# Optimization experiments

Hardware: AMD Instinct MI355X
Metric: run time of the kernel (lower is better)

Reference implementation:

```python
import jax, jax.numpy as jnp
import numpy as np

EPS = 1e-5

def _ln(x, g, b):
    m = jnp.mean(x, axis=-1, keepdims=True)
    v = jnp.var(x, axis=-1, keepdims=True)
    return (x - m) / jnp.sqrt(v + EPS) * g + b

def _mha(q, k, v, Wqkv, bqkv, Wo, bo, nh):
    # torch nn.MultiheadAttention with packed in_proj: rows [0:D]=Q, [D:2D]=K, [2D:3D]=V
    D = q.shape[-1]; hd = D // nh
    qp = q @ Wqkv[:D].T + bqkv[:D]
    kp = k @ Wqkv[D:2 * D].T + bqkv[D:2 * D]
    vp = v @ Wqkv[2 * D:].T + bqkv[2 * D:]
    sh = lambda t: t.reshape(t.shape[0], t.shape[1], nh, hd).transpose(0, 2, 1, 3)
    scores = jnp.einsum('bhqd,bhkd->bhqk', sh(qp), sh(kp)) / np.float32(np.sqrt(hd))
    a = jax.nn.softmax(scores, axis=-1)
    o = jnp.einsum('bhqk,bhkd->bhqd', a, sh(vp)).transpose(0, 2, 1, 3).reshape(q.shape[0], q.shape[1], D)
    return o @ Wo.T + bo

def _forward(x, W_in, b_in, W_l, b_l, g_l, be_l, W_ih, W_hh, b_ih, b_hh, mem0,
             W_rh, b_rh, W_wh, b_wh, W_eh, b_eh, W_rg, b_rg, W_wg, b_wg,
             W_wm_qkv, b_wm_qkv, W_wm_o, b_wm_o, W_ca_qkv, b_ca_qkv, W_ca_o, b_ca_o,
             W_ai, b_ai, g_ca, be_ca, W_out, b_out):
    B, S, _ = x.shape
    H = W_in.shape[0]
    # input projection + residual MLP stack (eval mode: dropout is identity)
    h = x @ W_in.T + b_in
    for i in range(W_l.shape[0]):
        r = h
        h = _ln(jax.nn.relu(h @ W_l[i].T + b_l[i]), g_l[i], be_l[i])
        h = h + r  # use_residual=True
    # working-memory (NTM-style) scan over time
    Hd = H

    def step(carry, xt):
        hs, cs, mem = carry
        gates = xt @ W_ih.T + b_ih + hs @ W_hh.T + b_hh
        i_, f_, g_, o_ = jnp.split(gates, 4, axis=-1)  # torch LSTM gate order i,f,g,o
        cs = jax.nn.sigmoid(f_) * cs + jax.nn.sigmoid(i_) * jnp.tanh(g_)
        hs = jax.nn.sigmoid(o_) * jnp.tanh(cs)
        # read (attention over memory, then gate)
        rk = hs @ W_rh.T + b_rh
        ro = _mha(rk[:, None, :], mem, mem, W_wm_qkv, b_wm_qkv, W_wm_o, b_wm_o, 4)
        rg = jax.nn.sigmoid(hs @ W_rg.T + b_rg)  # [B,1]
        read = (rg[:, :, None] * ro)[:, 0]
        # write (erase + add with content-based addressing, unscaled bmm softmax)
        wp = hs @ W_wh.T + b_wh
        wk, wv = wp[:, :Hd], wp[:, Hd:]
        ev = jax.nn.sigmoid(hs @ W_eh.T + b_eh)
        wg = jax.nn.sigmoid(hs @ W_wg.T + b_wg)  # [B,1]
        att = jax.nn.softmax(jnp.einsum('bd,bmd->bm', wk, mem), axis=-1)
        ew = att[:, :, None]  # [B,M,1]
        mem = mem * (1.0 - ew * ev[:, None, :]) + wg[:, None, :] * (ew * wv[:, None, :])
        return (hs, cs, mem), xt + read

    mem_init = jnp.broadcast_to(mem0, (B,) + mem0.shape)
    init = (jnp.zeros((B, H), x.dtype), jnp.zeros((B, H), x.dtype), mem_init)
    _, outs = jax.lax.scan(step, init, h.transpose(1, 0, 2))
    wm = outs.transpose(1, 0, 2)  # [B,S,H]
    # cognitive attention, task_type='general' (no task modulation branch)
    att = _mha(wm, wm, wm, W_ca_qkv, b_ca_qkv, W_ca_o, b_ca_o, 8)
    inten = jax.nn.sigmoid(wm @ W_ai.T + b_ai)
    co = _ln(att * inten + wm, g_ca, be_ca)
    return co @ W_out.T + b_out

def setup_inputs():
    key = jax.random.key(0)
    ks = iter(jax.random.split(key, 40))
    B, S, DI, H, DO, L, M = 16, 512, 64, 128, 64, 3, 32
    w = lambda *s: jax.random.normal(next(ks), s, jnp.float32) * 0.05
    d = {}
    d['x'] = jax.random.normal(next(ks), (B, S, DI), jnp.float32)
    d['W_in'] = w(H, DI); d['b_in'] = jnp.zeros(H)
    d['W_l'] = w(L, H, H); d['b_l'] = jnp.zeros((L, H))
    d['g_l'] = jnp.ones((L, H)); d['be_l'] = jnp.zeros((L, H))
    d['W_ih'] = w(4 * H, H); d['W_hh'] = w(4 * H, H)
    d['b_ih'] = jnp.zeros(4 * H); d['b_hh'] = jnp.zeros(4 * H)
    d['mem0'] = w(M, H)
    d['W_rh'] = w(H, H); d['b_rh'] = jnp.zeros(H)
    d['W_wh'] = w(2 * H, H); d['b_wh'] = jnp.zeros(2 * H)
    d['W_eh'] = w(H, H); d['b_eh'] = jnp.zeros(H)
    d['W_rg'] = w(1, H); d['b_rg'] = jnp.zeros(1)
    d['W_wg'] = w(1, H); d['b_wg'] = jnp.zeros(1)
    d['W_wm_qkv'] = w(3 * H, H); d['b_wm_qkv'] = jnp.zeros(3 * H)
    d['W_wm_o'] = w(H, H); d['b_wm_o'] = jnp.zeros(H)
    d['W_ca_qkv'] = w(3 * H, H); d['b_ca_qkv'] = jnp.zeros(3 * H)
    d['W_ca_o'] = w(H, H); d['b_ca_o'] = jnp.zeros(H)
    d['W_ai'] = w(1, H); d['b_ai'] = jnp.zeros(1)
    d['g_ca'] = jnp.ones(H); d['be_ca'] = jnp.zeros(H)
    d['W_out'] = w(DO, H); d['b_out'] = jnp.zeros(DO)
    return d

def reference(x, W_in, b_in, W_l, b_l, g_l, be_l, W_ih, W_hh, b_ih, b_hh, mem0,
              W_rh, b_rh, W_wh, b_wh, W_eh, b_eh, W_rg, b_rg, W_wg, b_wg,
              W_wm_qkv, b_wm_qkv, W_wm_o, b_wm_o, W_ca_qkv, b_ca_qkv, W_ca_o, b_ca_o,
              W_ai, b_ai, g_ca, be_ca, W_out, b_out):
    return _forward(x, W_in, b_in, W_l, b_l, g_l, be_l, W_ih, W_hh, b_ih, b_hh, mem0,
                    W_rh, b_rh, W_wh, b_wh, W_eh, b_eh, W_rg, b_rg, W_wg, b_wg,
                    W_wm_qkv, b_wm_qkv, W_wm_o, b_wm_o, W_ca_qkv, b_ca_qkv, W_ca_o, b_ca_o,
                    W_ai, b_ai, g_ca, be_ca, W_out, b_out)
```

## Files before the change

### kernel.cpp

```cpp
#include <hip/hip_runtime.h>
#include <hip/hip_bf16.h>


typedef short bf16x8 __attribute__((ext_vector_type(8)));
typedef float f32x4 __attribute__((ext_vector_type(4)));

__device__ __forceinline__ float bl(uint u) { return __uint_as_float(u << 16); }
__device__ __forceinline__ float bh(uint u) { return __uint_as_float(u & 0xffff0000u); }
__device__ __forceinline__ float b2f(ushort u) { return __uint_as_float(((uint)u) << 16); }
__device__ __forceinline__ ushort f2b(float f) {
  uint u = __float_as_uint(f);
  u += 0x7fffu + ((u >> 16) & 1u);
  return (ushort)(u >> 16);
}
__device__ __forceinline__ float rdl(float v, int lane) {
  return __int_as_float(__builtin_amdgcn_readlane(__float_as_int(v), lane));
}
__device__ __forceinline__ float sigm(float x) { return 1.0f / (1.0f + __expf(-x)); }
__device__ __forceinline__ float tanh_(float x) { float e = __expf(2.0f * x); return 1.0f - 2.0f / (e + 1.0f); }

#define O_H     ((size_t)0)
#define O_GX    ((size_t)1048576)
#define O_QCA   ((size_t)1048576)
#define O_KCA   ((size_t)2097152)
#define O_VCA   ((size_t)3145728)
#define O_AO    ((size_t)4194304)
#define O_HS    ((size_t)5242880)
#define O_WM    ((size_t)5242880)
#define O_WK    ((size_t)6291456)
#define O_WV    ((size_t)7340032)
#define O_EV    ((size_t)8388608)
#define O_Q     ((size_t)9437184)
#define O_WGS   ((size_t)10485760)
#define O_RGS   ((size_t)10493952)
#define O_BQC   ((size_t)10502144)
#define O_MEMA  ((size_t)10502272)
#define O_PWIN  ((size_t)27279488)
#define O_PWL   ((size_t)27283584)
#define O_PWIH  ((size_t)27308160)
#define O_PCMB  ((size_t)27340928)
#define O_PQKV  ((size_t)27373696)
#define O_PWOC  ((size_t)27398272)
#define O_PWOUT ((size_t)27406464)
#define O_PWOWM ((size_t)27410688)
#define O_WQC16 ((size_t)27418880)
#define O_CAN   ((size_t)27427072)

#define F4LD(DST, OFS, P) { float4 _f = *(const float4*)(P); DST[(OFS)]=_f.x; DST[(OFS)+1]=_f.y; DST[(OFS)+2]=_f.z; DST[(OFS)+3]=_f.w; }

struct CV { const void* src; uint dst; uint n; };
struct CVA { CV d[36]; };
__global__ __launch_bounds__(256) void k_cvt(CVA a, ushort* cb)
{
  __shared__ int flag;
  int tid = threadIdx.x;
  const ushort* xu = (const ushort*)a.d[0].src;
  if (tid < 64) {
    int sane = 0;
    for (int i = tid; i < 512; i += 64) {
      int e = (xu[2 * i] >> 7) & 0xFF;
      sane += (e >= 0x70 && e <= 0x8E) ? 1 : 0;
    }
#pragma unroll
    for (int d = 1; d < 64; d <<= 1) sane += __shfl_xor(sane, d, 64);
    if (tid == 0) flag = (sane > 256) ? 0 : 1;
  }
  __syncthreads();
  int isf32 = flag;
  CV c = a.d[blockIdx.x];
  ushort* dst = cb + c.dst;
  uint start = blockIdx.y * 256 + tid, stride = gridDim.y * 256;
  if (isf32) {
    const float* s = (const float*)c.src;
    for (uint j = start; j < c.n; j += stride) dst[j] = f2b(s[j]);
  } else {
    const ushort* s = (const ushort*)c.src;
    for (uint j = start; j < c.n; j += stride) dst[j] = s[j];
  }
}

__global__ __launch_bounds__(256) void k_wqcomb(const ushort* __restrict__ Wqkv, const ushort* __restrict__ Wrh,
                                                const ushort* __restrict__ brh, const ushort* __restrict__ bqkv,
                                                ushort* __restrict__ wqc, float* __restrict__ bqc)
{
  __shared__ float qr[2][128];
  int tid = threadIdx.x;
  int r = tid >> 7, e = tid & 127;
  int j = blockIdx.x * 2 + r;
  qr[r][e] = b2f(Wqkv[j * 128 + e]);
  __syncthreads();
  float acc = 0.f;
  for (int k = 0; k < 128; ++k) acc += qr[r][k] * b2f(Wrh[k * 128 + e]);
  wqc[j * 128 + e] = f2b(acc);
  if (e == 0) {
    float s = 0.f;
    for (int k = 0; k < 128; ++k) s += qr[r][k] * b2f(brh[k]);
    bqc[j] = s + b2f(bqkv[j]);
  }
}

struct PD { const ushort* src; uint* dst; int R, C2, RT, base; };
struct PA { PD d[12]; };
__global__ __launch_bounds__(256) void k_pack(PA a)
{
  int p = blockIdx.x >> 5, sl = blockIdx.x & 31;
  PD q = a.d[p];
  for (int d2 = sl; d2 < q.C2; d2 += 32)
    for (int j = threadIdx.x; j < q.R; j += 256)
      q.dst[(size_t)d2 * q.RT + q.base + j] = *(const uint*)(q.src + (size_t)j * q.C2 * 2 + d2 * 2);
}

__device__ __forceinline__ void mlp_layer(float& h0, float& h1, const uint* wp, const float* bias, int li, int l)
{
  float t0 = bias[(1 + li) * 128 + l], t1 = bias[(1 + li) * 128 + 64 + l];
// ... 47 lines not shown
    for (int d2 = 0; d2 < 32; ++d2) {
      float s0 = rdl(xv, 2 * d2), s1 = rdl(xv, 2 * d2 + 1);
      uint u0 = lds[d2 * 128 + l], u1 = lds[d2 * 128 + 64 + l];
      h0 += s0 * bl(u0) + s1 * bh(u0);
      h1 += s0 * bl(u1) + s1 * bh(u1);
    }
    mlp_layer(h0, h1, lds + 4096, bias, 0, l);
    h0a[ps] = h0; h1a[ps] = h1;
  }
  __syncthreads();
  for (int i = tid; i < 8192; i += 256) lds[i] = pk[12288 + i];
  __syncthreads();
#pragma unroll
  for (int ps = 0; ps < 8; ++ps) {
    float h0 = h0a[ps], h1 = h1a[ps];
    mlp_layer(h0, h1, lds, bias, 1, l);
    h0a[ps] = h0; h1a[ps] = h1;
  }
  __syncthreads();
  for (int i = tid; i < 8192; i += 256) lds[i] = pk[20480 + i];
  __syncthreads();
#pragma unroll
  for (int ps = 0; ps < 8; ++ps) {
    int tok = blockIdx.x * 32 + ps * 4 + wv;
    float h0 = h0a[ps], h1 = h1a[ps];
    mlp_layer(h0, h1, lds, bias, 2, l);
    h_all[(size_t)tok * 128 + l] = h0;
    h_all[(size_t)tok * 128 + 64 + l] = h1;
  }
}

__global__ __launch_bounds__(256, 1) void k_gates(const float* __restrict__ h_all, const uint* __restrict__ pk,
    const ushort* __restrict__ b_ih, const ushort* __restrict__ b_hh, float* __restrict__ gx)
{
  __shared__ uint lds[8192];
  __shared__ float biasg[512];
  int tid = threadIdx.x;
  for (int i = tid; i < 512; i += 256) biasg[i] = b2f(b_ih[i]) + b2f(b_hh[i]);
  int wv = tid >> 6, l = tid & 63;
  for (int s = 0; s < 4; ++s) {
    __syncthreads();
    for (int i = tid; i < 8192; i += 256) { int d2 = i >> 7, j = i & 127; lds[i] = pk[d2 * 512 + s * 128 + j]; }
    __syncthreads();
    for (int ps = 0; ps < 8; ++ps) {
      int tok = blockIdx.x * 32 + ps * 4 + wv;
      float h0 = h_all[(size_t)tok * 128 + l], h1 = h_all[(size_t)tok * 128 + 64 + l];
      float a0 = biasg[s * 128 + l], a1 = biasg[s * 128 + 64 + l];
#pragma unroll
      for (int d2 = 0; d2 < 64; ++d2) {
        float s0 = rdl(d2 < 32 ? h0 : h1, (2 * d2) & 63);
        float s1 = rdl(d2 < 32 ? h0 : h1, (2 * d2 + 1) & 63);
        uint u0 = lds[d2 * 128 + l], u1 = lds[d2 * 128 + 64 + l];
        a0 += s0 * bl(u0) + s1 * bh(u0);
        a1 += s0 * bl(u1) + s1 * bh(u1);
      }
      gx[(size_t)tok * 512 + s * 128 + l] = a0;
      gx[(size_t)tok * 512 + s * 128 + 64 + l] = a1;
    }
  }
}

__global__ __launch_bounds__(512, 2) void k_lstm(const float* __restrict__ gx, const ushort* __restrict__ Whh,
                                                 float* __restrict__ hs_all)
{
  __shared__ float hsl[128];
  __shared__ float gact[512];
  int tid = threadIdx.x;
  int b = blockIdx.x;
  float2 w2[64];
  {
    const ushort* rp = Whh + (size_t)tid * 128;
#pragma unroll
    for (int q = 0; q < 16; ++q) {
      uint4 v = *(const uint4*)(rp + q * 8);
      w2[q * 4 + 0] = make_float2(bl(v.x), bh(v.x));
      w2[q * 4 + 1] = make_float2(bl(v.y), bh(v.y));
      w2[q * 4 + 2] = make_float2(bl(v.z), bh(v.z));
      w2[q * 4 + 3] = make_float2(bl(v.w), bh(v.w));
    }
  }
  if (tid < 128) hsl[tid] = 0.f;
  float cs = 0.f;
  const float* gbase = gx + (size_t)b * 512 * 512;
  float gcur = gbase[tid];
  int grp = tid >> 7;
  __syncthreads();
  for (int t = 0; t < 512; ++t) {
    float gnext = 0.f;
    if (t < 511) gnext = gbase[(size_t)(t + 1) * 512 + tid];
    float ax = gcur, ay = 0.f;
#pragma unroll
    for (int i = 0; i < 64; ++i) {
      float2 s2 = *(const float2*)(hsl + 2 * i);
      ax = fmaf(w2[i].x, s2.x, ax);
      ay = fmaf(w2[i].y, s2.y, ay);
    }
    float a = ax + ay;
    gact[tid] = (grp == 2) ? tanh_(a) : sigm(a);
    __syncthreads();
    if (tid < 128) {
      float si = gact[tid], sf = gact[128 + tid], tg = gact[256 + tid], so = gact[384 + tid];
      cs = sf * cs + si * tg;
      float hv = so * tanh_(cs);
      hsl[tid] = hv;
      hs_all[((size_t)b * 512 + t) * 128 + tid] = hv;
    }
    gcur = gnext;
    __syncthreads();
  }
}

__global__ __launch_bounds__(256, 1) void k_proj(const float* __restrict__ hs_all, const uint* __restrict__ pk,
    const ushort* __restrict__ bwh, const ushort* __restrict__ beh, const float* __restrict__ bqc,
    const ushort* __restrict__ wrg, const ushort* __restrict__ brg, const ushort* __restrict__ wwg,
    const ushort* __restrict__ bwg,
    float* __restrict__ wk_a, float* __restrict__ wv_a, float* __restrict__ ev_a, float* __restrict__ q_a,
    float* __restrict__ rg_a, float* __restrict__ wg_a)
{
  __shared__ uint lds[8192];
  __shared__ float biasc[512];
  int tid = threadIdx.x;
  for (int i = tid; i < 512; i += 256)
    biasc[i] = (i < 256) ? b2f(bwh[i]) : (i < 384) ? b2f(beh[i - 256]) : bqc[i - 384];
  float brgv = b2f(brg[0]), bwgv = b2f(bwg[0]);
  int wv = tid >> 6, l = tid & 63;
  for (int s = 0; s < 4; ++s) {
    __syncthreads();
    for (int i = tid; i < 8192; i += 256) { int d2 = i >> 7, j = i & 127; lds[i] = pk[d2 * 512 + s * 128 + j]; }
    __syncthreads();
    for (int ps = 0; ps < 8; ++ps) {
      int tok = blockIdx.x * 32 + ps * 4 + wv;
      float h0 = hs_all[(size_t)tok * 128 + l], h1 = hs_all[(size_t)tok * 128 + 64 + l];
      float a0 = biasc[s * 128 + l], a1 = biasc[s * 128 + 64 + l];
#pragma unroll
      for (int d2 = 0; d2 < 64; ++d2) {
        float s0 = rdl(d2 < 32 ? h0 : h1, (2 * d2) & 63);
        float s1 = rdl(d2 < 32 ? h0 : h1, (2 * d2 + 1) & 63);
        uint u0 = lds[d2 * 128 + l], u1 = lds[d2 * 128 + 64 + l];
        a0 += s0 * bl(u0) + s1 * bh(u0);
        a1 += s0 * bl(u1) + s1 * bh(u1);
      }
      if (s == 0) {
        wk_a[(size_t)tok * 128 + l] = a0;
        wk_a[(size_t)tok * 128 + 64 + l] = a1;
        float pr = h0 * b2f(wrg[l]) + h1 * b2f(wrg[64 + l]);
        float pw = h0 * b2f(wwg[l]) + h1 * b2f(wwg[64 + l]);
#pragma unroll
        for (int d = 1; d < 64; d <<= 1) { pr += __shfl_xor(pr, d, 64); pw += __shfl_xor(pw, d, 64); }
        if (l == 0) { rg_a[tok] = sigm(pr + brgv); wg_a[tok] = sigm(pw + bwgv); }
      } else if (s == 1) {
        wv_a[(size_t)tok * 128 + l] = a0;
        wv_a[(size_t)tok * 128 + 64 + l] = a1;
      } else if (s == 2) {
        ev_a[(size_t)tok * 128 + l] = sigm(a0);
        ev_a[(size_t)tok * 128 + 64 + l] = sigm(a1);
      } else {
        q_a[(size_t)tok * 128 + l] = a0;
        q_a[(size_t)tok * 128 + 64 + l] = a1;
      }
    }
  }
}

#define B2STEP(T, CK, CV, CE, CG, NK, NV, NE, NG) { \
    { uint p0 = (uint)f2b(mr[0]) | ((uint)f2b(mr[1]) << 16); \
      uint p1 = (uint)f2b(mr[2]) | ((uint)f2b(mr[3]) << 16); \
      uint p2 = (uint)f2b(mr[4]) | ((uint)f2b(mr[5]) << 16); \
      uint p3 = (uint)f2b(mr[6]) | ((uint)f2b(mr[7]) << 16); \
      uint p4 = (uint)f2b(mr[8]) | ((uint)f2b(mr[9]) << 16); \
      uint p5 = (uint)f2b(mr[10]) | ((uint)f2b(mr[11]) << 16); \
      uint p6 = (uint)f2b(mr[12]) | ((uint)f2b(mr[13]) << 16); \
      uint p7 = (uint)f2b(mr[14]) | ((uint)f2b(mr[15]) << 16); \
      uint4* d4 = (uint4*)(mb + (size_t)(T) * 2048); \
      d4[0] = make_uint4(p0, p1, p2, p3); \
      d4[1] = make_uint4(p4, p5, p6, p7); } \
    if ((T) + 1 < 512) { \
      size_t nb = base0 + (size_t)((T) + 1) * 128; \
      F4LD(NK, 0, wk_a + nb); F4LD(NK, 4, wk_a + nb + 4); F4LD(NK, 8, wk_a + nb + 8); F4LD(NK, 12, wk_a + nb + 12); \
      F4LD(NV, 0, wv_a + nb); F4LD(NV, 4, wv_a + nb + 4); F4LD(NV, 8, wv_a + nb + 8); F4LD(NV, 12, wv_a + nb + 12); \
      F4LD(NE, 0, ev_a + nb); F4LD(NE, 4, ev_a + nb + 4); F4LD(NE, 8, ev_a + nb + 8); F4LD(NE, 12, ev_a + nb + 12); \
      NG = wg_a[(size_t)b * 512 + (T) + 1]; } \
    float dp = 0.f; \
    _Pragma("unroll") for (int i = 0; i < 16; ++i) dp += CK[i] * mr[i]; \
    dp += __shfl_xor(dp, 1, 64); dp += __shfl_xor(dp, 2, 64); dp += __shfl_xor(dp, 4, 64); \
    float mx = dp; \
    mx = fmaxf(mx, __shfl_xor(mx, 8, 64)); mx = fmaxf(mx, __shfl_xor(mx, 16, 64)); mx = fmaxf(mx, __shfl_xor(mx, 32, 64)); \
    if (l == 0) red[w] = mx; \
    __syncthreads(); \
    mx = fmaxf(fmaxf(red[0], red[1]), fmaxf(red[2], red[3])); \
    float e = __expf(dp - mx); \
    float smv = e; \
    smv += __shfl_xor(smv, 8, 64); smv += __shfl_xor(smv, 16, 64); smv += __shfl_xor(smv, 32, 64); \
    if (l == 0) red[4 + w] = smv; \
    __syncthreads(); \
    float den = (red[4] + red[5]) + (red[6] + red[7]); \
    float ew = e / den; \
    float gw = (CG) * ew; \
    _Pragma("unroll") for (int i = 0; i < 16; ++i) mr[i] = mr[i] * (1.f - ew * CE[i]) + gw * CV[i]; \
  }

__global__ __launch_bounds__(256, 1) void k_memrec(const float* __restrict__ wk_a, const float* __restrict__ wv_a,
    const float* __restrict__ ev_a, const float* __restrict__ wg_a, const ushort* __restrict__ mem0,
    uint* __restrict__ mem_all)
{
  __shared__ float red[8];
  int tid = threadIdx.x, l = tid & 63, w = tid >> 6;
  int b = blockIdx.x;
  int m = tid >> 3, d0 = (tid & 7) * 16;
  float mr[16];
#pragma unroll
  for (int i = 0; i < 16; ++i) mr[i] = b2f(mem0[m * 128 + d0 + i]);
  float ck[16], cv[16], ce[16], cg;
  float nk[16], nv[16], ne[16], ng;
  ng = 0.f; cg = 0.f;
  size_t base0 = (size_t)b * 512 * 128 + d0;
  F4LD(ck, 0, wk_a + base0); F4LD(ck, 4, wk_a + base0 + 4); F4LD(ck, 8, wk_a + base0 + 8); F4LD(ck, 12, wk_a + base0 + 12);
  F4LD(cv, 0, wv_a + base0); F4LD(cv, 4, wv_a + base0 + 4); F4LD(cv, 8, wv_a + base0 + 8); F4LD(cv, 12, wv_a + base0 + 12);
  F4LD(ce, 0, ev_a + base0); F4LD(ce, 4, ev_a + base0 + 4); F4LD(ce, 8, ev_a + base0 + 8); F4LD(ce, 12, ev_a + base0 + 12);
  cg = wg_a[(size_t)b * 512];
  uint* mb = mem_all + (size_t)b * 512 * 2048 + tid * 8;
  for (int t = 0; t < 512; t += 2) {
    B2STEP(t, ck, cv, ce, cg, nk, nv, ne, ng);
    B2STEP(t + 1, nk, nv, ne, ng, ck, cv, ce, cg);
  }
}

__global__ __launch_bounds__(256, 1) void k_read(const ushort* __restrict__ Wqkv, const ushort* __restrict__ bwo,
    const uint* __restrict__ wo_pk, const uint* __restrict__ mem_all, const float* __restrict__ q_all,
    const float* __restrict__ rg_all, const float* __restrict__ h_all, float* __restrict__ wm_all)
{
  __shared__ float Kl[32 * 133];
  __shared__ float Vl[32 * 133];
  __shared__ __align__(16) char ml[8192];
  __shared__ float ql[128];
  __shared__ float ol[128];
  __shared__ float part[256];
  int tid = threadIdx.x, l = tid & 63, w = tid >> 6;
  int b = blockIdx.x >> 6, c = blockIdx.x & 63;
  int mat = w >> 1, chh = w & 1;
  bf16x8 bfr[4][4];
#pragma unroll
  for (int ct = 0; ct < 4; ++ct)
#pragma unroll
    for (int kt = 0; kt < 4; ++kt) {
      int j = chh * 64 + ct * 16 + (l & 15);
      bfr[ct][kt] = *(const bf16x8*)(Wqkv + (size_t)(128 + mat * 128 + j) * 128 + kt * 32 + (l >> 4) * 8);
    }
  for (int s8 = 0; s8 < 8; ++s8) {
    int t = c * 8 + s8;
    size_t bt = (size_t)b * 512 + t;
    {
      const uint4* src = (const uint4*)(mem_all + bt * 2048);
      uint4 v0 = src[tid * 2], v1 = src[tid * 2 + 1];
      int row = tid >> 3;
      int b0 = row * 256 + (tid & 7) * 32;
      int sw = (row & 7) << 4;
      *(uint4*)(ml + (b0 ^ sw)) = v0;
      *(uint4*)(ml + ((b0 + 16) ^ sw)) = v1;
    }
    if (tid < 128) ql[tid] = q_all[bt * 128 + tid];
    __syncthreads();
    f32x4 acc[2][4];
#pragma unroll
    for (int rt = 0; rt < 2; ++rt)
#pragma unroll
      for (int ct = 0; ct < 4; ++ct) { f32x4 z = {0.f, 0.f, 0.f, 0.f}; acc[rt][ct] = z; }
    bf16x8 af[2][4];
#pragma unroll
    for (int rt = 0; rt < 2; ++rt)
#pragma unroll
      for (int kt = 0; kt < 4; ++kt) {
        int row = rt * 16 + (l & 15);
        int byte0 = (row * 256 + kt * 64 + (l >> 4) * 16) ^ ((row & 7) << 4);
        af[rt][kt] = *(const bf16x8*)(ml + byte0);
      }
#pragma unroll
    for (int rt = 0; rt < 2; ++rt)
#pragma unroll
      for (int ct = 0; ct < 4; ++ct)
#pragma unroll
        for (int kt = 0; kt < 4; ++kt)
          acc[rt][ct] = __builtin_amdgcn_mfma_f32_16x16x32_bf16(af[rt][kt], bfr[ct][kt], acc[rt][ct], 0, 0, 0);
    {
      float* dst = mat ? Vl : Kl;
#pragma unroll
      for (int rt = 0; rt < 2; ++rt)
#pragma unroll
        for (int ct = 0; ct < 4; ++ct)
#pragma unroll
          for (int rr = 0; rr < 4; ++rr) {
            int row = rt * 16 + (l >> 4) * 4 + rr;
            int col = chh * 64 + ct * 16 + (l & 15);
            dst[row * 133 + col] = acc[rt][ct][rr];
          }
    }
    __syncthreads();
    {
      int hh = w;
      float qv[16];
#pragma unroll
      for (int q = 0; q < 4; ++q) { F4LD(qv, 4 * q, ql + hh * 32 + (l >> 5) * 16 + 4 * q); }
      int m = l & 31;
      float sv = 0.f;
#pragma unroll
      for (int i = 0; i < 16; ++i) sv += qv[i] * Kl[m * 133 + hh * 32 + (l >> 5) * 16 + i];
      sv += __shfl_xor(sv, 32, 64);
// ... 201 lines not shown
      float s1 = rdl(d2 < 32 ? c0 : c1, (2 * d2 + 1) & 63);
      uint u = lds[8192 + d2 * 64 + l];
      ob += s0 * bl(u) + s1 * bh(u);
    }
    out[(size_t)tok * 64 + l] = ob;
  }
}

extern "C" void kernel_launch(void* const* d_in, const int* in_sizes, int n_in,
                              void* d_out, int out_size, void* d_ws, size_t ws_size,
                              hipStream_t stream)
{
  (void)out_size; (void)ws_size;
  float* ws = (float*)d_ws;
  uint* wsu = (uint*)d_ws;
  ushort* cb = (ushort*)(wsu + O_CAN);

  uint off[36]; uint cum = 0;
  for (int i = 0; i < 36; ++i) { off[i] = cum; cum = (cum + (uint)in_sizes[i] + 7u) & ~7u; }

  CVA ca;
  for (int i = 0; i < 36; ++i) ca.d[i] = CV{ d_in[i], off[i], (uint)in_sizes[i] };
  k_cvt<<<dim3(36, 16), 256, 0, stream>>>(ca, cb);

  const ushort* x        = cb + off[0];
  const ushort* W_in     = cb + off[1];
  const ushort* b_in     = cb + off[2];
  const ushort* W_l      = cb + off[3];
  const ushort* b_l      = cb + off[4];
  const ushort* g_l      = cb + off[5];
  const ushort* be_l     = cb + off[6];
  const ushort* W_ih     = cb + off[7];
  const ushort* W_hh     = cb + off[8];
  const ushort* b_ih     = cb + off[9];
  const ushort* b_hh     = cb + off[10];
  const ushort* mem0     = cb + off[11];
  const ushort* W_rh     = cb + off[12];
  const ushort* b_rh     = cb + off[13];
  const ushort* W_wh     = cb + off[14];
  const ushort* b_wh     = cb + off[15];
  const ushort* W_eh     = cb + off[16];
  const ushort* b_eh     = cb + off[17];
  const ushort* W_rg     = cb + off[18];
  const ushort* b_rg     = cb + off[19];
  const ushort* W_wg     = cb + off[20];
  const ushort* b_wg     = cb + off[21];
  const ushort* W_wm_qkv = cb + off[22];
  const ushort* b_wm_qkv = cb + off[23];
  const ushort* W_wm_o   = cb + off[24];
  const ushort* b_wm_o   = cb + off[25];
  const ushort* W_ca_qkv = cb + off[26];
  const ushort* b_ca_qkv = cb + off[27];
  const ushort* W_ca_o   = cb + off[28];
  const ushort* b_ca_o   = cb + off[29];
  const ushort* W_ai     = cb + off[30];
  const ushort* b_ai     = cb + off[31];
  const ushort* g_ca     = cb + off[32];
  const ushort* be_ca    = cb + off[33];
  const ushort* W_out    = cb + off[34];
  const ushort* b_out    = cb + off[35];

  k_wqcomb<<<64, 256, 0, stream>>>(W_wm_qkv, W_rh, b_rh, b_wm_qkv, (ushort*)(wsu + O_WQC16), ws + O_BQC);

  PA pa;
  pa.d[0]  = PD{ W_in,                       wsu + O_PWIN,  128, 32, 128, 0 };
  pa.d[1]  = PD{ W_l,                        wsu + O_PWL,   128, 64, 128, 0 };
  pa.d[2]  = PD{ W_l + 16384,                wsu + O_PWL + 8192,  128, 64, 128, 0 };
  pa.d[3]  = PD{ W_l + 32768,                wsu + O_PWL + 16384, 128, 64, 128, 0 };
  pa.d[4]  = PD{ W_ih,                       wsu + O_PWIH,  512, 64, 512, 0 };
  pa.d[5]  = PD{ W_wh,                       wsu + O_PCMB,  256, 64, 512, 0 };
  pa.d[6]  = PD{ W_eh,                       wsu + O_PCMB,  128, 64, 512, 256 };
  pa.d[7]  = PD{ (const ushort*)(wsu + O_WQC16), wsu + O_PCMB, 128, 64, 512, 384 };
  pa.d[8]  = PD{ W_ca_qkv,                   wsu + O_PQKV,  384, 64, 384, 0 };
  pa.d[9]  = PD{ W_ca_o,                     wsu + O_PWOC,  128, 64, 128, 0 };
  pa.d[10] = PD{ W_out,                      wsu + O_PWOUT,  64, 64,  64, 0 };
  pa.d[11] = PD{ W_wm_o,                     wsu + O_PWOWM, 128, 64, 128, 0 };
  k_pack<<<384, 256, 0, stream>>>(pa);

  k_mlp<<<256, 256, 0, stream>>>(x, wsu + O_PWIN, b_in, b_l, g_l, be_l, ws + O_H);
  k_gates<<<256, 256, 0, stream>>>(ws + O_H, wsu + O_PWIH, b_ih, b_hh, ws + O_GX);
  k_lstm<<<16, 512, 0, stream>>>(ws + O_GX, W_hh, ws + O_HS);
  k_proj<<<256, 256, 0, stream>>>(ws + O_HS, wsu + O_PCMB, b_wh, b_eh, ws + O_BQC,
                                  W_rg, b_rg, W_wg, b_wg,
                                  ws + O_WK, ws + O_WV, ws + O_EV, ws + O_Q, ws + O_RGS, ws + O_WGS);
  k_memrec<<<16, 256, 0, stream>>>(ws + O_WK, ws + O_WV, ws + O_EV, ws + O_WGS, mem0, wsu + O_MEMA);
  k_read<<<1024, 256, 0, stream>>>(W_wm_qkv, b_wm_o, wsu + O_PWOWM, wsu + O_MEMA,
                                   ws + O_Q, ws + O_RGS, ws + O_H, ws + O_WM);
  k_caqkv<<<256, 256, 0, stream>>>(ws + O_WM, wsu + O_PQKV, b_ca_qkv, ws + O_QCA, ws + O_KCA, ws + O_VCA);
  k_caattn<<<256, 256, 0, stream>>>(ws + O_QCA, ws + O_KCA, ws + O_VCA, ws + O_AO);
  k_cafinal<<<256, 256, 0, stream>>>(ws + O_WM, ws + O_AO, wsu + O_PWOC, wsu + O_PWOUT,
                                     W_ai, b_ai, g_ca, be_ca, b_ca_o, b_out, (float*)d_out);
}
```

Before: 1.543 ms.

## Rewrite memory recurrence as single-wave kernel; batch LSTM hidden-state stores

The memory-update recurrence kernel moves from 256 threads with two block barriers per step to a single 64-lane wave. Each lane owns two feature columns across all 32 memory slots, uses a shuffle-based transpose reduction for the slot scores, and packs bf16 with a hardware convert instruction. This removes the per-step __syncthreads cost on the serial 512-step path, at the price of more work per lane and lower parallelism. The LSTM kernel also buffers eight hidden states and prefetches eight gate rows at a time, batching its global stores.

```diff
diff --git a/kernel.cpp b/kernel.cpp
--- a/kernel.cpp
+++ b/kernel.cpp
@@ -12,6 +12,11 @@
   uint u = __float_as_uint(f);
   u += 0x7fffu + ((u >> 16) & 1u);
   return (ushort)(u >> 16);
+}
+__device__ __forceinline__ uint cvtpk(float lo, float hi) {
+  uint r;
+  asm("v_cvt_pk_bf16_f32 %0, %1, %2" : "=v"(r) : "v"(lo), "v"(hi));
+  return r;
 }
 __device__ __forceinline__ float rdl(float v, int lane) {
   return __int_as_float(__builtin_amdgcn_readlane(__float_as_int(v), lane));
@@ -243,31 +248,44 @@
   if (tid < 128) hsl[tid] = 0.f;
   float cs = 0.f;
   const float* gbase = gx + (size_t)b * 512 * 512;
-  float gcur = gbase[tid];
   int grp = tid >> 7;
-  __syncthreads();
-  for (int t = 0; t < 512; ++t) {
-    float gnext = 0.f;
-    if (t < 511) gnext = gbase[(size_t)(t + 1) * 512 + tid];
-    float ax = gcur, ay = 0.f;
-#pragma unroll
-    for (int i = 0; i < 64; ++i) {
-      float2 s2 = *(const float2*)(hsl + 2 * i);
-      ax = fmaf(w2[i].x, s2.x, ax);
-      ay = fmaf(w2[i].y, s2.y, ay);
-    }
-    float a = ax + ay;
-    gact[tid] = (grp == 2) ? tanh_(a) : sigm(a);
-    __syncthreads();
+  float g8[8], g8n[8], hv8[8];
+#pragma unroll
+  for (int j = 0; j < 8; ++j) { g8[j] = gbase[(size_t)j * 512 + tid]; hv8[j] = 0.f; g8n[j] = 0.f; }
+  __syncthreads();
+  for (int tb = 0; tb < 512; tb += 8) {
+    if (tb + 8 < 512) {
+#pragma unroll
+      for (int j = 0; j < 8; ++j) g8n[j] = gbase[(size_t)(tb + 8 + j) * 512 + tid];
+    }
+#pragma unroll
+    for (int j = 0; j < 8; ++j) {
+      float ax = g8[j], ay = 0.f;
+#pragma unroll
+      for (int i = 0; i < 64; ++i) {
+        float2 s2 = *(const float2*)(hsl + 2 * i);
+        ax = fmaf(w2[i].x, s2.x, ax);
+        ay = fmaf(w2[i].y, s2.y, ay);
+      }
+      float a = ax + ay;
+      gact[tid] = (grp == 2) ? tanh_(a) : sigm(a);
+      __syncthreads();
+      if (tid < 128) {
+        float si = gact[tid], sf = gact[128 + tid], tg = gact[256 + tid], so = gact[384 + tid];
+        cs = sf * cs + si * tg;
+        float hv = so * tanh_(cs);
+        hsl[tid] = hv;
+        hv8[j] = hv;
+      }
+      __syncthreads();
+    }
     if (tid < 128) {
-      float si = gact[tid], sf = gact[128 + tid], tg = gact[256 + tid], so = gact[384 + tid];
-      cs = sf * cs + si * tg;
-      float hv = so * tanh_(cs);
-      hsl[tid] = hv;
-      hs_all[((size_t)b * 512 + t) * 128 + tid] = hv;
-    }
-    gcur = gnext;
-    __syncthreads();
+      float* hp = hs_all + ((size_t)b * 512 + tb) * 128 + tid;
+#pragma unroll
+      for (int j = 0; j < 8; ++j) hp[(size_t)j * 128] = hv8[j];
+    }
+#pragma unroll
+    for (int j = 0; j < 8; ++j) g8[j] = g8n[j];
   }
 }
 
@@ -323,66 +341,91 @@
   }
 }
 
-#define B2STEP(T, CK, CV, CE, CG, NK, NV, NE, NG) { \
-    { uint p0 = (uint)f2b(mr[0]) | ((uint)f2b(mr[1]) << 16); \
-      uint p1 = (uint)f2b(mr[2]) | ((uint)f2b(mr[3]) << 16); \
-      uint p2 = (uint)f2b(mr[4]) | ((uint)f2b(mr[5]) << 16); \
-      uint p3 = (uint)f2b(mr[6]) | ((uint)f2b(mr[7]) << 16); \
-      uint p4 = (uint)f2b(mr[8]) | ((uint)f2b(mr[9]) << 16); \
-      uint p5 = (uint)f2b(mr[10]) | ((uint)f2b(mr[11]) << 16); \
-      uint p6 = (uint)f2b(mr[12]) | ((uint)f2b(mr[13]) << 16); \
-      uint p7 = (uint)f2b(mr[14]) | ((uint)f2b(mr[15]) << 16); \
-      uint4* d4 = (uint4*)(mb + (size_t)(T) * 2048); \
-      d4[0] = make_uint4(p0, p1, p2, p3); \
-      d4[1] = make_uint4(p4, p5, p6, p7); } \
-    if ((T) + 1 < 512) { \
-      size_t nb = base0 + (size_t)((T) + 1) * 128; \
-      F4LD(NK, 0, wk_a + nb); F4LD(NK, 4, wk_a + nb + 4); F4LD(NK, 8, wk_a + nb + 8); F4LD(NK, 12, wk_a + nb + 12); \
-      F4LD(NV, 0, wv_a + nb); F4LD(NV, 4, wv_a + nb + 4); F4LD(NV, 8, wv_a + nb + 8); F4LD(NV, 12, wv_a + nb + 12); \
-      F4LD(NE, 0, ev_a + nb); F4LD(NE, 4, ev_a + nb + 4); F4LD(NE, 8, ev_a + nb + 8); F4LD(NE, 12, ev_a + nb + 12); \
-      NG = wg_a[(size_t)b * 512 + (T) + 1]; } \
-    float dp = 0.f; \
-    _Pragma("unroll") for (int i = 0; i < 16; ++i) dp += CK[i] * mr[i]; \
-    dp += __shfl_xor(dp, 1, 64); dp += __shfl_xor(dp, 2, 64); dp += __shfl_xor(dp, 4, 64); \
-    float mx = dp; \
-    mx = fmaxf(mx, __shfl_xor(mx, 8, 64)); mx = fmaxf(mx, __shfl_xor(mx, 16, 64)); mx = fmaxf(mx, __shfl_xor(mx, 32, 64)); \
-    if (l == 0) red[w] = mx; \
-    __syncthreads(); \
-    mx = fmaxf(fmaxf(red[0], red[1]), fmaxf(red[2], red[3])); \
-    float e = __expf(dp - mx); \
-    float smv = e; \
-    smv += __shfl_xor(smv, 8, 64); smv += __shfl_xor(smv, 16, 64); smv += __shfl_xor(smv, 32, 64); \
-    if (l == 0) red[4 + w] = smv; \
-    __syncthreads(); \
-    float den = (red[4] + red[5]) + (red[6] + red[7]); \
-    float ew = e / den; \
-    float gw = (CG) * ew; \
-    _Pragma("unroll") for (int i = 0; i < 16; ++i) mr[i] = mr[i] * (1.f - ew * CE[i]) + gw * CV[i]; \
-  }
-
-__global__ __launch_bounds__(256, 1) void k_memrec(const float* __restrict__ wk_a, const float* __restrict__ wv_a,
+__global__ __launch_bounds__(64, 1) void k_memrec(const float* __restrict__ wk_a, const float* __restrict__ wv_a,
     const float* __restrict__ ev_a, const float* __restrict__ wg_a, const ushort* __restrict__ mem0,
     uint* __restrict__ mem_all)
 {
-  __shared__ float red[8];
-  int tid = threadIdx.x, l = tid & 63, w = tid >> 6;
+  __shared__ float ewl[64];
+  int l = threadIdx.x;
   int b = blockIdx.x;
-  int m = tid >> 3, d0 = (tid & 7) * 16;
-  float mr[16];
-#pragma unroll
-  for (int i = 0; i < 16; ++i) mr[i] = b2f(mem0[m * 128 + d0 + i]);
-  float ck[16], cv[16], ce[16], cg;
-  float nk[16], nv[16], ne[16], ng;
-  ng = 0.f; cg = 0.f;
-  size_t base0 = (size_t)b * 512 * 128 + d0;
-  F4LD(ck, 0, wk_a + base0); F4LD(ck, 4, wk_a + base0 + 4); F4LD(ck, 8, wk_a + base0 + 8); F4LD(ck, 12, wk_a + base0 + 12);
-  F4LD(cv, 0, wv_a + base0); F4LD(cv, 4, wv_a + base0 + 4); F4LD(cv, 8, wv_a + base0 + 8); F4LD(cv, 12, wv_a + base0 + 12);
-  F4LD(ce, 0, ev_a + base0); F4LD(ce, 4, ev_a + base0 + 4); F4LD(ce, 8, ev_a + base0 + 8); F4LD(ce, 12, ev_a + base0 + 12);
-  cg = wg_a[(size_t)b * 512];
-  uint* mb = mem_all + (size_t)b * 512 * 2048 + tid * 8;
-  for (int t = 0; t < 512; t += 2) {
-    B2STEP(t, ck, cv, ce, cg, nk, nv, ne, ng);
-    B2STEP(t + 1, nk, nv, ne, ng, ck, cv, ce, cg);
+  float mr0[32], mr1[32];
+  {
+    const uint* m0 = (const uint*)mem0;
+#pragma unroll
+    for (int m = 0; m < 32; ++m) { uint u = m0[m * 64 + l]; mr0[m] = bl(u); mr1[m] = bh(u); }
+  }
+  const float* wkp = wk_a + (size_t)b * 512 * 128 + 2 * l;
+  const float* wvp = wv_a + (size_t)b * 512 * 128 + 2 * l;
+  const float* evp = ev_a + (size_t)b * 512 * 128 + 2 * l;
+  const float* wgp = wg_a + (size_t)b * 512;
+  float2 cwk = *(const float2*)(wkp);
+  float2 cwv = *(const float2*)(wvp);
+  float2 cev = *(const float2*)(evp);
+  float cg = wgp[0];
+  uint* mb = mem_all + (size_t)b * 512 * 2048 + l;
+  for (int t = 0; t < 512; ++t) {
+    float2 nwk = make_float2(0.f, 0.f), nwv = nwk, nev = nwk;
+    float ng = 0.f;
+    if (t < 511) {
+      nwk = *(const float2*)(wkp + (size_t)(t + 1) * 128);
+      nwv = *(const float2*)(wvp + (size_t)(t + 1) * 128);
+      nev = *(const float2*)(evp + (size_t)(t + 1) * 128);
+      ng = wgp[t + 1];
+    }
+    {
+      uint* mt = mb + (size_t)t * 2048;
+#pragma unroll
+      for (int m = 0; m < 32; ++m) mt[m * 64] = cvtpk(mr0[m], mr1[m]);
+    }
+    float p[32];
+#pragma unroll
+    for (int m = 0; m < 32; ++m) p[m] = fmaf(cwk.x, mr0[m], cwk.y * mr1[m]);
+#pragma unroll
+    for (int m = 0; m < 32; ++m) p[m] += __shfl_xor(p[m], 32, 64);
+#define RSTAGE(S, HALF) { bool hb = (l & (S)) != 0; \
+    _Pragma("unroll") for (int i = 0; i < (HALF); ++i) { \
+      float send = hb ? p[i] : p[i + (HALF)]; \
+      float got = __shfl_xor(send, (S), 64); \
+      float keep = hb ? p[i + (HALF)] : p[i]; \
+      p[i] = keep + got; } }
+    RSTAGE(16, 16)
+    RSTAGE(8, 8)
+    RSTAGE(4, 4)
+    RSTAGE(2, 2)
+    RSTAGE(1, 1)
+#undef RSTAGE
+    float dp = p[0];
+    float mx = dp;
+    mx = fmaxf(mx, __shfl_xor(mx, 1, 64));
+    mx = fmaxf(mx, __shfl_xor(mx, 2, 64));
+    mx = fmaxf(mx, __shfl_xor(mx, 4, 64));
+    mx = fmaxf(mx, __shfl_xor(mx, 8, 64));
+    mx = fmaxf(mx, __shfl_xor(mx, 16, 64));
+    float e = __expf(dp - mx);
+    float den = e;
+    den += __shfl_xor(den, 1, 64);
+    den += __shfl_xor(den, 2, 64);
+    den += __shfl_xor(den, 4, 64);
+    den += __shfl_xor(den, 8, 64);
+    den += __shfl_xor(den, 16, 64);
+    float ew = e / den;
+    ewl[l] = ew;
+    asm volatile("s_waitcnt lgkmcnt(0)" ::: "memory");
+    float gv0 = cg * cwv.x, gv1 = cg * cwv.y;
+#pragma unroll
+    for (int q = 0; q < 8; ++q) {
+      float4 e4 = *(const float4*)(ewl + 4 * q);
+      float ews[4] = { e4.x, e4.y, e4.z, e4.w };
+#pragma unroll
+      for (int r = 0; r < 4; ++r) {
+        int m = 4 * q + r;
+        float u0 = fmaf(-cev.x, mr0[m], gv0);
+        mr0[m] = fmaf(ews[r], u0, mr0[m]);
+        float u1 = fmaf(-cev.y, mr1[m], gv1);
+        mr1[m] = fmaf(ews[r], u1, mr1[m]);
+      }
+    }
+    cwk = nwk; cwv = nwv; cev = nev; cg = ng;
   }
 }
 
@@ -751,7 +794,7 @@
   k_proj<<<256, 256, 0, stream>>>(ws + O_HS, wsu + O_PCMB, b_wh, b_eh, ws + O_BQC,
                                   W_rg, b_rg, W_wg, b_wg,
                                   ws + O_WK, ws + O_WV, ws + O_EV, ws + O_Q, ws + O_RGS, ws + O_WGS);
-  k_memrec<<<16, 256, 0, stream>>>(ws + O_WK, ws + O_WV, ws + O_EV, ws + O_WGS, mem0, wsu + O_MEMA);
+  k_memrec<<<16, 64, 0, stream>>>(ws + O_WK, ws + O_WV, ws + O_EV, ws + O_WGS, mem0, wsu + O_MEMA);
   k_read<<<1024, 256, 0, stream>>>(W_wm_qkv, b_wm_o, wsu + O_PWOWM, wsu + O_MEMA,
                                    ws + O_Q, ws + O_RGS, ws + O_H, ws + O_WM);
   k_caqkv<<<256, 256, 0, stream>>>(ws + O_WM, wsu + O_PQKV, b_ca_qkv, ws + O_QCA, ws + O_KCA, ws + O_VCA);
```

Result: slower. 2.127 ms (+37.9%).

## Rewrite memory recurrence as single-wavefront kernel with DPP reductions and lagged softmax max

Applied to the files above, without the earlier changes.

The sequential memory-write scan moves from a 256-thread block to one 64-lane wavefront per batch. Each lane holds half a memory row (64 floats), so the block-wide __syncthreads and LDS max/sum reductions are replaced by DPP row-rotates and ds_swizzle. The per-step inputs are packed into one interleaved buffer, with the write gate pre-multiplied into wv, and double-buffered through LDS. Bf16 packing uses v_cvt_pk_bf16_f32. The softmax offset is the previous step's max rather than the current one, with a clamp on the denominator, which risks overflow or underflow if the scores move sharply between steps.

```diff
diff --git a/kernel.cpp b/kernel.cpp
--- a/kernel.cpp
+++ b/kernel.cpp
@@ -13,11 +13,40 @@
   u += 0x7fffu + ((u >> 16) & 1u);
   return (ushort)(u >> 16);
 }
+__device__ __forceinline__ uint cvtpk(float lo, float hi) {
+  uint r;
+  asm("v_cvt_pk_bf16_f32 %0, %1, %2" : "=v"(r) : "v"(lo), "v"(hi));
+  return r;
+}
 __device__ __forceinline__ float rdl(float v, int lane) {
   return __int_as_float(__builtin_amdgcn_readlane(__float_as_int(v), lane));
 }
 __device__ __forceinline__ float sigm(float x) { return 1.0f / (1.0f + __expf(-x)); }
 __device__ __forceinline__ float tanh_(float x) { float e = __expf(2.0f * x); return 1.0f - 2.0f / (e + 1.0f); }
+
+__device__ __forceinline__ float dppror_add(float v, const int n) {
+  int s;
+  switch (n) {
+    case 1: s = __builtin_amdgcn_update_dpp(0, __float_as_int(v), 0x121, 0xF, 0xF, true); break;
+    case 2: s = __builtin_amdgcn_update_dpp(0, __float_as_int(v), 0x122, 0xF, 0xF, true); break;
+    case 4: s = __builtin_amdgcn_update_dpp(0, __float_as_int(v), 0x124, 0xF, 0xF, true); break;
+    default: s = __builtin_amdgcn_update_dpp(0, __float_as_int(v), 0x128, 0xF, 0xF, true); break;
+  }
+  return v + __int_as_float(s);
+}
+__device__ __forceinline__ float dppror_max(float v, const int n) {
+  int s;
+  switch (n) {
+    case 1: s = __builtin_amdgcn_update_dpp(0, __float_as_int(v), 0x121, 0xF, 0xF, true); break;
+    case 2: s = __builtin_amdgcn_update_dpp(0, __float_as_int(v), 0x122, 0xF, 0xF, true); break;
+    case 4: s = __builtin_amdgcn_update_dpp(0, __float_as_int(v), 0x124, 0xF, 0xF, true); break;
+    default: s = __builtin_amdgcn_update_dpp(0, __float_as_int(v), 0x128, 0xF, 0xF, true); break;
+  }
+  return fmaxf(v, __int_as_float(s));
+}
+__device__ __forceinline__ float swz16(float v) {
+  return __int_as_float(__builtin_amdgcn_ds_swizzle(__float_as_int(v), 0x401F));
+}
 
 #define O_H     ((size_t)0)
 #define O_GX    ((size_t)1048576)
@@ -27,9 +56,7 @@
 #define O_AO    ((size_t)4194304)
 #define O_HS    ((size_t)5242880)
 #define O_WM    ((size_t)5242880)
-#define O_WK    ((size_t)6291456)
-#define O_WV    ((size_t)7340032)
-#define O_EV    ((size_t)8388608)
+#define O_ST    ((size_t)6291456)
 #define O_Q     ((size_t)9437184)
 #define O_WGS   ((size_t)10485760)
 #define O_RGS   ((size_t)10493952)
@@ -275,8 +302,7 @@
     const ushort* __restrict__ bwh, const ushort* __restrict__ beh, const float* __restrict__ bqc,
     const ushort* __restrict__ wrg, const ushort* __restrict__ brg, const ushort* __restrict__ wwg,
     const ushort* __restrict__ bwg,
-    float* __restrict__ wk_a, float* __restrict__ wv_a, float* __restrict__ ev_a, float* __restrict__ q_a,
-    float* __restrict__ rg_a, float* __restrict__ wg_a)
+    float* __restrict__ st, float* __restrict__ q_a, float* __restrict__ rg_a)
 {
   __shared__ uint lds[8192];
   __shared__ float biasc[512];
@@ -302,19 +328,22 @@
         a1 += s0 * bl(u1) + s1 * bh(u1);
       }
       if (s == 0) {
-        wk_a[(size_t)tok * 128 + l] = a0;
-        wk_a[(size_t)tok * 128 + 64 + l] = a1;
+        st[(size_t)tok * 384 + l] = a0;
+        st[(size_t)tok * 384 + 64 + l] = a1;
         float pr = h0 * b2f(wrg[l]) + h1 * b2f(wrg[64 + l]);
+#pragma unroll
+        for (int d = 1; d < 64; d <<= 1) pr += __shfl_xor(pr, d, 64);
+        if (l == 0) rg_a[tok] = sigm(pr + brgv);
+      } else if (s == 1) {
         float pw = h0 * b2f(wwg[l]) + h1 * b2f(wwg[64 + l]);
 #pragma unroll
-        for (int d = 1; d < 64; d <<= 1) { pr += __shfl_xor(pr, d, 64); pw += __shfl_xor(pw, d, 64); }
-        if (l == 0) { rg_a[tok] = sigm(pr + brgv); wg_a[tok] = sigm(pw + bwgv); }
-      } else if (s == 1) {
-        wv_a[(size_t)tok * 128 + l] = a0;
-        wv_a[(size_t)tok * 128 + 64 + l] = a1;
+        for (int d = 1; d < 64; d <<= 1) pw += __shfl_xor(pw, d, 64);
+        float wg = sigm(pw + bwgv);
+        st[(size_t)tok * 384 + 256 + l] = wg * a0;
+        st[(size_t)tok * 384 + 256 + 64 + l] = wg * a1;
       } else if (s == 2) {
-        ev_a[(size_t)tok * 128 + l] = sigm(a0);
-        ev_a[(size_t)tok * 128 + 64 + l] = sigm(a1);
+        st[(size_t)tok * 384 + 128 + l] = sigm(a0);
+        st[(size_t)tok * 384 + 128 + 64 + l] = sigm(a1);
       } else {
         q_a[(size_t)tok * 128 + l] = a0;
         q_a[(size_t)tok * 128 + 64 + l] = a1;
@@ -323,66 +352,91 @@
   }
 }
 
-#define B2STEP(T, CK, CV, CE, CG, NK, NV, NE, NG) { \
-    { uint p0 = (uint)f2b(mr[0]) | ((uint)f2b(mr[1]) << 16); \
-      uint p1 = (uint)f2b(mr[2]) | ((uint)f2b(mr[3]) << 16); \
-      uint p2 = (uint)f2b(mr[4]) | ((uint)f2b(mr[5]) << 16); \
-      uint p3 = (uint)f2b(mr[6]) | ((uint)f2b(mr[7]) << 16); \
-      uint p4 = (uint)f2b(mr[8]) | ((uint)f2b(mr[9]) << 16); \
-      uint p5 = (uint)f2b(mr[10]) | ((uint)f2b(mr[11]) << 16); \
-      uint p6 = (uint)f2b(mr[12]) | ((uint)f2b(mr[13]) << 16); \
-      uint p7 = (uint)f2b(mr[14]) | ((uint)f2b(mr[15]) << 16); \
-      uint4* d4 = (uint4*)(mb + (size_t)(T) * 2048); \
-      d4[0] = make_uint4(p0, p1, p2, p3); \
-      d4[1] = make_uint4(p4, p5, p6, p7); } \
-    if ((T) + 1 < 512) { \
-      size_t nb = base0 + (size_t)((T) + 1) * 128; \
-      F4LD(NK, 0, wk_a + nb); F4LD(NK, 4, wk_a + nb + 4); F4LD(NK, 8, wk_a + nb + 8); F4LD(NK, 12, wk_a + nb + 12); \
-      F4LD(NV, 0, wv_a + nb); F4LD(NV, 4, wv_a + nb + 4); F4LD(NV, 8, wv_a + nb + 8); F4LD(NV, 12, wv_a + nb + 12); \
-      F4LD(NE, 0, ev_a + nb); F4LD(NE, 4, ev_a + nb + 4); F4LD(NE, 8, ev_a + nb + 8); F4LD(NE, 12, ev_a + nb + 12); \
-      NG = wg_a[(size_t)b * 512 + (T) + 1]; } \
-    float dp = 0.f; \
-    _Pragma("unroll") for (int i = 0; i < 16; ++i) dp += CK[i] * mr[i]; \
-    dp += __shfl_xor(dp, 1, 64); dp += __shfl_xor(dp, 2, 64); dp += __shfl_xor(dp, 4, 64); \
-    float mx = dp; \
-    mx = fmaxf(mx, __shfl_xor(mx, 8, 64)); mx = fmaxf(mx, __shfl_xor(mx, 16, 64)); mx = fmaxf(mx, __shfl_xor(mx, 32, 64)); \
-    if (l == 0) red[w] = mx; \
-    __syncthreads(); \
-    mx = fmaxf(fmaxf(red[0], red[1]), fmaxf(red[2], red[3])); \
-    float e = __expf(dp - mx); \
-    float smv = e; \
-    smv += __shfl_xor(smv, 8, 64); smv += __shfl_xor(smv, 16, 64); smv += __shfl_xor(smv, 32, 64); \
-    if (l == 0) red[4 + w] = smv; \
-    __syncthreads(); \
-    float den = (red[4] + red[5]) + (red[6] + red[7]); \
-    float ew = e / den; \
-    float gw = (CG) * ew; \
-    _Pragma("unroll") for (int i = 0; i < 16; ++i) mr[i] = mr[i] * (1.f - ew * CE[i]) + gw * CV[i]; \
-  }
-
-__global__ __launch_bounds__(256, 1) void k_memrec(const float* __restrict__ wk_a, const float* __restrict__ wv_a,
-    const float* __restrict__ ev_a, const float* __restrict__ wg_a, const ushort* __restrict__ mem0,
+__global__ __launch_bounds__(64, 1) void k_memrec(const float* __restrict__ st, const ushort* __restrict__ mem0,
     uint* __restrict__ mem_all)
 {
-  __shared__ float red[8];
-  int tid = threadIdx.x, l = tid & 63, w = tid >> 6;
+  __shared__ __align__(16) float sbuf[2][384];
+  int l = threadIdx.x;
   int b = blockIdx.x;
-  int m = tid >> 3, d0 = (tid & 7) * 16;
-  float mr[16];
-#pragma unroll
-  for (int i = 0; i < 16; ++i) mr[i] = b2f(mem0[m * 128 + d0 + i]);
-  float ck[16], cv[16], ce[16], cg;
-  float nk[16], nv[16], ne[16], ng;
-  ng = 0.f; cg = 0.f;
-  size_t base0 = (size_t)b * 512 * 128 + d0;
-  F4LD(ck, 0, wk_a + base0); F4LD(ck, 4, wk_a + base0 + 4); F4LD(ck, 8, wk_a + base0 + 8); F4LD(ck, 12, wk_a + base0 + 12);
-  F4LD(cv, 0, wv_a + base0); F4LD(cv, 4, wv_a + base0 + 4); F4LD(cv, 8, wv_a + base0 + 8); F4LD(cv, 12, wv_a + base0 + 12);
-  F4LD(ce, 0, ev_a + base0); F4LD(ce, 4, ev_a + base0 + 4); F4LD(ce, 8, ev_a + base0 + 8); F4LD(ce, 12, ev_a + base0 + 12);
-  cg = wg_a[(size_t)b * 512];
-  uint* mb = mem_all + (size_t)b * 512 * 2048 + tid * 8;
-  for (int t = 0; t < 512; t += 2) {
-    B2STEP(t, ck, cv, ce, cg, nk, nv, ne, ng);
-    B2STEP(t + 1, nk, nv, ne, ng, ck, cv, ce, cg);
+  int r = l & 31, h = l >> 5;
+  float2 m2[32];
+  {
+    const uint* m0 = (const uint*)mem0 + r * 64 + 32 * h;
+#pragma unroll
+    for (int q = 0; q < 8; ++q) {
+      uint4 u = *(const uint4*)(m0 + 4 * q);
+      m2[4 * q + 0] = make_float2(bl(u.x), bh(u.x));
+      m2[4 * q + 1] = make_float2(bl(u.y), bh(u.y));
+      m2[4 * q + 2] = make_float2(bl(u.z), bh(u.z));
+      m2[4 * q + 3] = make_float2(bl(u.w), bh(u.w));
+    }
+  }
+  const float* stb = st + (size_t)b * 512 * 384;
+  {
+    float4 a = *(const float4*)(stb + 4 * l);
+    float2 c = *(const float2*)(stb + 256 + 2 * l);
+    *(float4*)(&sbuf[0][4 * l]) = a;
+    *(float2*)(&sbuf[0][256 + 2 * l]) = c;
+  }
+  float moff = 0.f;
+  uint* mbase = mem_all + (size_t)b * 512 * 2048 + (size_t)r * 64 + 32 * h;
+  for (int t = 0; t < 512; ++t) {
+    int cur = t & 1, nxt = cur ^ 1;
+    float4 ga = make_float4(0.f, 0.f, 0.f, 0.f);
+    float2 gc = make_float2(0.f, 0.f);
+    if (t < 511) {
+      const float* sp = stb + (size_t)(t + 1) * 384;
+      ga = *(const float4*)(sp + 4 * l);
+      gc = *(const float2*)(sp + 256 + 2 * l);
+    }
+    {
+      uint* mt = mbase + (size_t)t * 2048;
+#pragma unroll
+      for (int q = 0; q < 8; ++q) {
+        uint4 v;
+        v.x = cvtpk(m2[4 * q + 0].x, m2[4 * q + 0].y);
+        v.y = cvtpk(m2[4 * q + 1].x, m2[4 * q + 1].y);
+        v.z = cvtpk(m2[4 * q + 2].x, m2[4 * q + 2].y);
+        v.w = cvtpk(m2[4 * q + 3].x, m2[4 * q + 3].y);
+        *(uint4*)(mt + 4 * q) = v;
+      }
+    }
+    const float* wkp = &sbuf[cur][h * 64];
+    float dx = 0.f, dy = 0.f, dz = 0.f, dw = 0.f;
+#pragma unroll
+    for (int j = 0; j < 16; ++j) {
+      float4 w4 = *(const float4*)(wkp + 4 * j);
+      dx = fmaf(w4.x, m2[2 * j].x, dx);
+      dy = fmaf(w4.y, m2[2 * j].y, dy);
+      dz = fmaf(w4.z, m2[2 * j + 1].x, dz);
+      dw = fmaf(w4.w, m2[2 * j + 1].y, dw);
+    }
+    float dp = (dx + dy) + (dz + dw);
+    dp += __shfl_xor(dp, 32, 64);
+    float e = __expf(dp - moff);
+    float s16 = dppror_add(dppror_add(dppror_add(dppror_add(e, 1), 2), 4), 8);
+    float den = s16 + swz16(s16);
+    den = fmaxf(den, 1e-30f);
+    float ew = e / den;
+    float x16 = dppror_max(dppror_max(dppror_max(dppror_max(dp, 1), 2), 4), 8);
+    const float* evp = &sbuf[cur][128 + h * 64];
+    const float* gvp = &sbuf[cur][256 + h * 64];
+#pragma unroll
+    for (int j = 0; j < 16; ++j) {
+      float4 e4 = *(const float4*)(evp + 4 * j);
+      float4 g4 = *(const float4*)(gvp + 4 * j);
+      float2 a = m2[2 * j], c = m2[2 * j + 1];
+      a.x = fmaf(ew, fmaf(-e4.x, a.x, g4.x), a.x);
+      a.y = fmaf(ew, fmaf(-e4.y, a.y, g4.y), a.y);
+      c.x = fmaf(ew, fmaf(-e4.z, c.x, g4.z), c.x);
+      c.y = fmaf(ew, fmaf(-e4.w, c.y, g4.w), c.y);
+      m2[2 * j] = a; m2[2 * j + 1] = c;
+    }
+    if (t < 511) {
+      *(float4*)(&sbuf[nxt][4 * l]) = ga;
+      *(float2*)(&sbuf[nxt][256 + 2 * l]) = gc;
+    }
+    moff = fmaxf(x16, swz16(x16));
   }
 }
 
@@ -750,8 +804,8 @@
   k_lstm<<<16, 512, 0, stream>>>(ws + O_GX, W_hh, ws + O_HS);
   k_proj<<<256, 256, 0, stream>>>(ws + O_HS, wsu + O_PCMB, b_wh, b_eh, ws + O_BQC,
                                   W_rg, b_rg, W_wg, b_wg,
-                                  ws + O_WK, ws + O_WV, ws + O_EV, ws + O_Q, ws + O_RGS, ws + O_WGS);
-  k_memrec<<<16, 256, 0, stream>>>(ws + O_WK, ws + O_WV, ws + O_EV, ws + O_WGS, mem0, wsu + O_MEMA);
+                                  ws + O_ST, ws + O_Q, ws + O_RGS);
+  k_memrec<<<16, 64, 0, stream>>>(ws + O_ST, mem0, wsu + O_MEMA);
   k_read<<<1024, 256, 0, stream>>>(W_wm_qkv, b_wm_o, wsu + O_PWOWM, wsu + O_MEMA,
                                    ws + O_Q, ws + O_RGS, ws + O_H, ws + O_WM);
   k_caqkv<<<256, 256, 0, stream>>>(ws + O_WM, wsu + O_PQKV, b_ca_qkv, ws + O_QCA, ws + O_KCA, ws + O_VCA);
```

New measurement: 1.709 ms. +10.8%, slower.
